# Kernel tuning notes

Measured on AMD Instinct MI355X. Metric: run time of the kernel, lower is better.

## Reference

```python
import jax, jax.numpy as jnp
import numpy as np

L0, L1, L2, L3 = 300000, 60000, 15000, 4000
E0, E1, E2 = 960000, 240000, 64000
F_IN, F_HID, F_OUT = 256, 128, 47


def setup_inputs() -> dict:
    key = jax.random.key(0)
    ks = jax.random.split(key, 12)
    return {
        "features": jax.random.normal(ks[0], (L0, F_IN), dtype=jnp.float32),
        "src0": jax.random.randint(ks[1], (E0,), 0, L0, dtype=jnp.int32),
        "dst0": jax.random.randint(ks[2], (E0,), 0, L1, dtype=jnp.int32),
        "src1": jax.random.randint(ks[3], (E1,), 0, L1, dtype=jnp.int32),
        "dst1": jax.random.randint(ks[4], (E1,), 0, L2, dtype=jnp.int32),
        "src2": jax.random.randint(ks[5], (E2,), 0, L2, dtype=jnp.int32),
        "dst2": jax.random.randint(ks[6], (E2,), 0, L3, dtype=jnp.int32),
        "W1": jax.random.normal(ks[7], (F_IN, F_HID), dtype=jnp.float32) * (1.0 / np.sqrt(F_IN)),
        "b1": jnp.zeros((F_HID,), dtype=jnp.float32),
        "W2": jax.random.normal(ks[8], (F_HID, F_HID), dtype=jnp.float32) * (1.0 / np.sqrt(F_HID)),
        "b2": jnp.zeros((F_HID,), dtype=jnp.float32),
        "W3": jax.random.normal(ks[9], (F_HID, F_OUT), dtype=jnp.float32) * (1.0 / np.sqrt(F_HID)),
        "b3": jnpp if False else jnp.zeros((F_OUT,), dtype=jnp.float32),
    }


def mean_agg(h, src, dst, n_dst):
    # copy_src gather over edges, then segment-mean over dst nodes
    msg = h[src]                                              # [E, F]
    s = jax.ops.segment_sum(msg, dst, num_segments=n_dst)     # [n_dst, F]
    cnt = jax.ops.segment_sum(jnp.ones_like(dst, dtype=h.dtype), dst, num_segments=n_dst)
    return s / jnp.maximum(cnt, 1.0)[:, None]


def reference(features, src0, dst0, src1, dst1, src2, dst2, W1, b1, W2, b2, W3, b3):
    # layer 0 -> 1: mean agg + linear + relu
    h = jax.nn.relu(mean_agg(features, src0, dst0, L1) @ W1 + b1)
    # layer 1 -> 2: mean agg + linear + relu
    h = jax.nn.relu(mean_agg(h, src1, dst1, L2) @ W2 + b2)
    # layer 2 -> 3: mean agg + linear (no activation on output layer)
    h = mean_agg(h, src2, dst2, L3) @ W3 + b3
    return h
```

## Files before the change

### kernel.cpp

```cpp
#include <hip/hip_runtime.h>

#define NL0 300000
#define NL1 60000
#define NL2 15000
#define NL3 4000
#define NE0 960000
#define NE1 240000
#define NE2 64000
#define E_ALL (NE0 + NE1 + NE2)
#define F_IN 256
#define F_HID 128
#define F_OUT 47

#define RBASE1 NL1
#define RBASE2 (NL1 + NL2)
#define NROWS (NL1 + NL2 + NL3)

#define FILL_BLOCKS ((E_ALL + 255) / 256)
#define WPREP_BLOCKS ((F_IN * F_HID) / 256)

typedef __attribute__((ext_vector_type(8))) short short8v;
typedef __attribute__((ext_vector_type(4))) float f32x4;

__device__ inline int wave_incl_scan(int v) {
    int lane = threadIdx.x & 63;
#pragma unroll
    for (int off = 1; off < 64; off <<= 1) {
        int t = __shfl_up(v, off, 64);
        if (lane >= off) v += t;
    }
    return v;
}

__device__ inline void bf16_split(float x, unsigned short& hi, unsigned short& lo) {
    unsigned int u = __float_as_uint(x);
    hi = (unsigned short)(u >> 16);
    float fh = __uint_as_float(u & 0xffff0000u);
    float l = x - fh;
    lo = (unsigned short)(__float_as_uint(l) >> 16);
}

__global__ void histogram_all(const int* __restrict__ dst0, const int* __restrict__ dst1,
                              const int* __restrict__ dst2, int* __restrict__ cnt) {
    int i = blockIdx.x * blockDim.x + threadIdx.x;
    if (i >= E_ALL) return;
    int k;
    if (i < NE0) {
        k = dst0[i];
    } else if (i < NE0 + NE1) {
        k = RBASE1 + dst1[i - NE0];
    } else {
        k = RBASE2 + dst2[i - NE0 - NE1];
    }
    atomicAdd(&cnt[k], 1);
}

__global__ __launch_bounds__(1024) void scan_block(const int* __restrict__ cnt, int N,
                                                   int* __restrict__ row_start,
                                                   int* __restrict__ blocksum) {
    __shared__ int wsum[16];
    int i = blockIdx.x * 1024 + threadIdx.x;
    int lane = threadIdx.x & 63, wid = threadIdx.x >> 6;
    int v = (i < N) ? cnt[i] : 0;
    int incl = wave_incl_scan(v);
    if (lane == 63) wsum[wid] = incl;
    __syncthreads();
    if (threadIdx.x < 16) {
        int w = wsum[threadIdx.x];
#pragma unroll
        for (int off = 1; off < 16; off <<= 1) {
            int t = __shfl_up(w, off, 64);
            if ((int)threadIdx.x >= off) w += t;
        }
        wsum[threadIdx.x] = w;
    }
    __syncthreads();
    int woff = wid ? wsum[wid - 1] : 0;
    if (i < N) row_start[i] = woff + incl - v;
    if (threadIdx.x == 0) blocksum[blockIdx.x] = wsum[15];
}

__global__ __launch_bounds__(1024) void add_offsets2(int* __restrict__ row_start,
                                                     const int* __restrict__ bs, int N, int E,
                                                     int* __restrict__ cursor) {
    __shared__ int soff;
    if (threadIdx.x < 64) {
        int s = 0;
        for (int j = threadIdx.x; j < blockIdx.x; j += 64) s += bs[j];
#pragma unroll
        for (int o = 32; o >= 1; o >>= 1) s += __shfl_xor(s, o, 64);
        if (threadIdx.x == 0) soff = s;
    }
    __syncthreads();
    int i = blockIdx.x * 1024 + threadIdx.x;
    if (i < N) {
        int v = row_start[i] + soff;
        row_start[i] = v;
        cursor[i] = v;
    }
    if (i == 0) row_start[N] = E;
}

__global__ void fill_all(const int* __restrict__ src0, const int* __restrict__ dst0,
                         const int* __restrict__ src1, const int* __restrict__ dst1,
                         const int* __restrict__ src2, const int* __restrict__ dst2,
                         int* __restrict__ cursor, int* __restrict__ ss,
                         const float* __restrict__ W1,
                         unsigned short* __restrict__ Whi,
                         unsigned short* __restrict__ Wlo) {
    int b = blockIdx.x;
    if (b >= FILL_BLOCKS) {
        int idx = (b - FILL_BLOCKS) * 256 + threadIdx.x;
        int k = idx >> 7, c = idx & 127;
        unsigned short h, l;
        bf16_split(W1[idx], h, l);
        Whi[c * 256 + k] = h;
        Wlo[c * 256 + k] = l;
        return;
    }
    int i = b * 256 + threadIdx.x;
    if (i >= E_ALL) return;
    int k, s;
    if (i < NE0) {
        s = src0[i];
        k = dst0[i];
    } else if (i < NE0 + NE1) {
        int e = i - NE0;
        s = src1[e];
        k = RBASE1 + dst1[e];
    } else {
        int e = i - NE0 - NE1;
        s = src2[e];
        k = RBASE2 + dst2[e];
    }
    int p = atomicAdd(&cursor[k], 1);
    ss[p] = s;
}

__global__ __launch_bounds__(256) void gather256(const float* __restrict__ h,
                                                 const int* __restrict__ rs,
                                                 const int* __restrict__ ss,
                                                 unsigned short* __restrict__ mhi,
                                                 unsigned short* __restrict__ mlo) {
    int lane = threadIdx.x & 63;
    int r = blockIdx.x * 4 + (threadIdx.x >> 6);
    if (r >= NL1) return;
    int s0 = rs[r], s1 = rs[r + 1];
    int tot = s1 - s0;

    const float* hp = h + (size_t)lane * 4;
    float4 acc0 = make_float4(0.f, 0.f, 0.f, 0.f);
    float4 acc1 = make_float4(0.f, 0.f, 0.f, 0.f);
    int e = s0;
    for (; e + 7 < s1; e += 8) {
        int i0 = ss[e], i1 = ss[e + 1], i2 = ss[e + 2], i3 = ss[e + 3];
        int i4 = ss[e + 4], i5 = ss[e + 5], i6 = ss[e + 6], i7 = ss[e + 7];
        float4 v0 = *(const float4*)(hp + (size_t)i0 * F_IN);
        float4 v1 = *(const float4*)(hp + (size_t)i1 * F_IN);
        float4 v2 = *(const float4*)(hp + (size_t)i2 * F_IN);
        float4 v3 = *(const float4*)(hp + (size_t)i3 * F_IN);
        float4 v4 = *(const float4*)(hp + (size_t)i4 * F_IN);
        float4 v5 = *(const float4*)(hp + (size_t)i5 * F_IN);
        float4 v6 = *(const float4*)(hp + (size_t)i6 * F_IN);
        float4 v7 = *(const float4*)(hp + (size_t)i7 * F_IN);
        acc0.x += (v0.x + v1.x) + (v2.x + v3.x);
        acc0.y += (v0.y + v1.y) + (v2.y + v3.y);
        acc0.z += (v0.z + v1.z) + (v2.z + v3.z);
        acc0.w += (v0.w + v1.w) + (v2.w + v3.w);
        acc1.x += (v4.x + v5.x) + (v6.x + v7.x);
        acc1.y += (v4.y + v5.y) + (v6.y + v7.y);
        acc1.z += (v4.z + v5.z) + (v6.z + v7.z);
        acc1.w += (v4.w + v5.w) + (v6.w + v7.w);
    }
    for (; e + 1 < s1; e += 2) {
        int i0 = ss[e], i1 = ss[e + 1];
        float4 v0 = *(const float4*)(hp + (size_t)i0 * F_IN);
        float4 v1 = *(const float4*)(hp + (size_t)i1 * F_IN);
        acc0.x += v0.x + v1.x; acc0.y += v0.y + v1.y;
        acc0.z += v0.z + v1.z; acc0.w += v0.w + v1.w;
    }
    if (e < s1) {
        int i0 = ss[e];
        float4 v0 = *(const float4*)(hp + (size_t)i0 * F_IN);
        acc0.x += v0.x; acc0.y += v0.y; acc0.z += v0.z; acc0.w += v0.w;
    }
    float inv = (tot > 0) ? 1.0f / (float)tot : 0.0f;
    float o[4] = {(acc0.x + acc1.x) * inv, (acc0.y + acc1.y) * inv,
                  (acc0.z + acc1.z) * inv, (acc0.w + acc1.w) * inv};
    ushort4 hv, lv;
    bf16_split(o[0], hv.x, lv.x);
    bf16_split(o[1], hv.y, lv.y);
    bf16_split(o[2], hv.z, lv.z);
    bf16_split(o[3], hv.w, lv.w);
    *(ushort4*)(mhi + (size_t)r * F_IN + lane * 4) = hv;
    *(ushort4*)(mlo + (size_t)r * F_IN + lane * 4) = lv;
}

__global__ __launch_bounds__(1024) void mfma_lin0(const unsigned short* __restrict__ Ahi,
                                                  const unsigned short* __restrict__ Alo,
                                                  const unsigned short* __restrict__ Whi,
                                                  const unsigned short* __restrict__ Wlo,
                                                  const float* __restrict__ bias,
                                                  float* __restrict__ out, int N) {
    __shared__ unsigned short whi[F_IN * F_HID];
    __shared__ unsigned short wlo[F_IN * F_HID];

    for (int ci = threadIdx.x; ci < (F_IN * F_HID) / 8; ci += 1024) {
        int e = ci * 8;
        int c = e >> 8;
        int swz = e ^ ((c & 7) << 3);
        *(short8v*)(whi + swz) = *(const short8v*)(Whi + e);
        *(short8v*)(wlo + swz) = *(const short8v*)(Wlo + e);
    }
    __syncthreads();

    int lane = threadIdx.x & 63;
    int wid = threadIdx.x >> 6;
    int rowbase = blockIdx.x * 256 + wid * 16;
    int r = lane & 15;
    int kg = lane >> 4;

    size_t arow = (size_t)min(rowbase + r, N - 1);
    const unsigned short* pah = Ahi + arow * F_IN + kg * 8;
    const unsigned short* pal = Alo + arow * F_IN + kg * 8;

    f32x4 acc[8];
#pragma unroll
    for (int ct = 0; ct < 8; ++ct) acc[ct] = (f32x4){0.f, 0.f, 0.f, 0.f};

#pragma unroll
    for (int ks = 0; ks < 8; ++ks) {
        short8v ah = *(const short8v*)(pah + ks * 32);
        short8v al = *(const short8v*)(pal + ks * 32);
#pragma unroll
        for (int ct = 0; ct < 8; ++ct) {
            int e = (((ct * 16 + r) << 8) + ks * 32 + kg * 8) ^ ((r & 7) << 3);
            short8v bh = *(const short8v*)(whi + e);
            short8v bl = *(const short8v*)(wlo + e);
            acc[ct] = __builtin_amdgcn_mfma_f32_16x16x32_bf16(ah, bh, acc[ct], 0, 0, 0);
            acc[ct] = __builtin_amdgcn_mfma_f32_16x16x32_bf16(ah, bl, acc[ct], 0, 0, 0);
            acc[ct] = __builtin_amdgcn_mfma_f32_16x16x32_bf16(al, bh, acc[ct], 0, 0, 0);
        }
    }

    int crow = rowbase + kg * 4;
#pragma unroll
    for (int ct = 0; ct < 8; ++ct) {
        float bb = bias[ct * 16 + r];
#pragma unroll
        for (int i = 0; i < 4; ++i) {
            int rr = crow + i;
            if (rr < N) out[(size_t)rr * F_HID + ct * 16 + r] = fmaxf(acc[ct][i] + bb, 0.f);
        }
    }
}

template <int FOUT, int ROWS, bool RELU>
__global__ __launch_bounds__(256) void gather_linear(const float* __restrict__ h,
                                                     const int* __restrict__ rs,
                                                     const int* __restrict__ ss,
                                                     const float* __restrict__ W,
                                                     const float* __restrict__ bias,
                                                     float* __restrict__ out,
                                                     int N, int rowbase) {
    __shared__ float mr[ROWS][128];

    int lane = threadIdx.x & 63;
    int w = threadIdx.x >> 6;
    int half = lane >> 5;
    int hl = lane & 31;
    int rb = blockIdx.x * ROWS;
    constexpr int RPW = ROWS / 4;
#pragma unroll
    for (int q = 0; q < RPW; ++q) {
        int lr = w * RPW + q;
        int r = rb + lr;
        float4 acc = make_float4(0.f, 0.f, 0.f, 0.f);
        if (r < N) {
            int s0 = rs[rowbase + r], s1 = rs[rowbase + r + 1];
            const float* hp = h + (size_t)hl * 4;
            int e = s0;
            for (; e + 3 < s1; e += 4) {
                int i0 = ss[e + half], i1 = ss[e + 2 + half];
                float4 v0 = *(const float4*)(hp + (size_t)i0 * F_HID);
                float4 v1 = *(const float4*)(hp + (size_t)i1 * F_HID);
                acc.x += v0.x + v1.x; acc.y += v0.y + v1.y;
                acc.z += v0.z + v1.z; acc.w += v0.w + v1.w;
            }
            if (e + 1 < s1) {
                int i0 = ss[e + half];
                float4 v0 = *(const float4*)(hp + (size_t)i0 * F_HID);
                acc.x += v0.x; acc.y += v0.y; acc.z += v0.z; acc.w += v0.w;
                e += 2;
            }
            if (e < s1 && half == 0) {
                int i0 = ss[e];
                float4 v0 = *(const float4*)(hp + (size_t)i0 * F_HID);
                acc.x += v0.x; acc.y += v0.y; acc.z += v0.z; acc.w += v0.w;
            }
            acc.x += __shfl(acc.x, lane ^ 32);
            acc.y += __shfl(acc.y, lane ^ 32);
            acc.z += __shfl(acc.z, lane ^ 32);
            acc.w += __shfl(acc.w, lane ^ 32);
            float inv = (s1 > s0) ? 1.0f / (float)(s1 - s0) : 0.0f;
            acc.x *= inv; acc.y *= inv; acc.z *= inv; acc.w *= inv;
        }
        if (half == 0) *(float4*)&mr[lr][hl * 4] = acc;
    }
    __syncthreads();

    if constexpr (FOUT == 128) {
        int c4 = (threadIdx.x & 31) * 4;
        int r0 = (threadIdx.x >> 5) & 7;
        float4 bb = *(const float4*)&bias[c4];
        float4 a0 = bb, a1 = bb;
#pragma unroll 8
        for (int k = 0; k < 128; ++k) {
            float4 wv = *(const float4*)&W[k * 128 + c4];
            float m0 = mr[r0][k];
            float m1 = mr[r0 + 8][k];
            a0.x += m0 * wv.x; a0.y += m0 * wv.y; a0.z += m0 * wv.z; a0.w += m0 * wv.w;
            a1.x += m1 * wv.x; a1.y += m1 * wv.y; a1.z += m1 * wv.z; a1.w += m1 * wv.w;
        }
        if (RELU) {
            a0.x = fmaxf(a0.x, 0.f); a0.y = fmaxf(a0.y, 0.f);
            a0.z = fmaxf(a0.z, 0.f); a0.w = fmaxf(a0.w, 0.f);
            a1.x = fmaxf(a1.x, 0.f); a1.y = fmaxf(a1.y, 0.f);
            a1.z = fmaxf(a1.z, 0.f); a1.w = fmaxf(a1.w, 0.f);
        }
        int ra = rb + r0, rb2 = rb + r0 + 8;
        if (ra < N) *(float4*)&out[(size_t)ra * 128 + c4] = a0;
        if (rb2 < N) *(float4*)&out[(size_t)rb2 * 128 + c4] = a1;
    } else {
        int j = lane;
        int rg = w;
        if (j < FOUT) {
            float bb = bias[j];
            float a0 = bb, a1 = bb;
#pragma unroll 8
            for (int k = 0; k < 128; ++k) {
                float wv = W[k * FOUT + j];
                a0 += mr[rg][k] * wv;
                a1 += mr[rg + 4][k] * wv;
            }
            if (RELU) { a0 = fmaxf(a0, 0.f); a1 = fmaxf(a1, 0.f); }
            int ra = rb + rg, rb2 = rb + rg + 4;
            if (ra < N) out[(size_t)ra * FOUT + j] = a0;
            if (rb2 < N) out[(size_t)rb2 * FOUT + j] = a1;
        }
    }
}


static inline size_t align256(size_t x) { return (x + 255) & ~size_t(255); }

extern "C" void kernel_launch(void* const* d_in, const int* in_sizes, int n_in,
                              void* d_out, int out_size, void* d_ws, size_t ws_size,
                              hipStream_t stream) {
    const float* features = (const float*)d_in[0];
    const int*   src0     = (const int*)d_in[1];
    const int*   dst0     = (const int*)d_in[2];
    const int*   src1     = (const int*)d_in[3];
    const int*   dst1     = (const int*)d_in[4];
    const int*   src2     = (const int*)d_in[5];
    const int*   dst2     = (const int*)d_in[6];
    const float* W1       = (const float*)d_in[7];
    const float* b1       = (const float*)d_in[8];
    const float* W2       = (const float*)d_in[9];
    const float* b2       = (const float*)d_in[10];
    const float* W3       = (const float*)d_in[11];
    const float* b3       = (const float*)d_in[12];
    float* out = (float*)d_out;

    char* p = (char*)d_ws;
    size_t off = 0;
    auto alloc = [&](size_t bytes) {
        char* r = p + off;
        off += align256(bytes);
        return r;
    };
    unsigned short* m0hi = (unsigned short*)alloc(sizeof(unsigned short) * (size_t)NL1 * F_IN);
    unsigned short* m0lo = (unsigned short*)alloc(sizeof(unsigned short) * (size_t)NL1 * F_IN);
    unsigned short* wt_hi = (unsigned short*)alloc(sizeof(unsigned short) * F_IN * F_HID);
    unsigned short* wt_lo = (unsigned short*)alloc(sizeof(unsigned short) * F_IN * F_HID);
    float* h1 = (float*)alloc(sizeof(float) * (size_t)NL1 * F_HID);
    float* h2 = (float*)alloc(sizeof(float) * (size_t)NL2 * F_HID);
    int* cnt = (int*)alloc(sizeof(int) * NROWS);
    int* rs  = (int*)alloc(sizeof(int) * (NROWS + 1));
    int* cur = (int*)alloc(sizeof(int) * NROWS);
    int* bs  = (int*)alloc(sizeof(int) * 1024);
    int* ss  = (int*)alloc(sizeof(int) * E_ALL);
    (void)ws_size;

    hipMemsetAsync(cnt, 0, sizeof(int) * NROWS, stream);
    histogram_all<<<(E_ALL + 255) / 256, 256, 0, stream>>>(dst0, dst1, dst2, cnt);
    int nb = (NROWS + 1023) / 1024;
    scan_block<<<nb, 1024, 0, stream>>>(cnt, NROWS, rs, bs);
    add_offsets2<<<nb, 1024, 0, stream>>>(rs, bs, NROWS, E_ALL, cur);
    fill_all<<<FILL_BLOCKS + WPREP_BLOCKS, 256, 0, stream>>>(
        src0, dst0, src1, dst1, src2, dst2, cur, ss, W1, wt_hi, wt_lo);

    gather256<<<NL1 / 4, 256, 0, stream>>>(features, rs, ss, m0hi, m0lo);
    mfma_lin0<<<(NL1 + 255) / 256, 1024, 0, stream>>>(m0hi, m0lo, wt_hi, wt_lo, b1, h1, NL1);

    gather_linear<128, 16, true><<<(NL2 + 15) / 16, 256, 0, stream>>>(
        h1, rs, ss, W2, b2, h2, NL2, RBASE1);

    gather_linear<F_OUT, 8, false><<<(NL3 + 7) / 8, 256, 0, stream>>>(
        h2, rs, ss, W3, b3, out, NL3, RBASE2);
}
```

Measured before the change: 372.7 us.

## Build CSR with partitioned counters and precomputed ranks instead of atomic fill

Replaces the histogram plus atomic-cursor fill with a count pass that records each edge's rank within one of eight per-partition counters, then places edges deterministically from per-partition bases. This removes the second round of atomics in the fill kernel and spreads counter contention across eight copies. In exchange it adds an 8x larger counter array to memset and scan, an extra rank array of E_ALL ints to write and read, and more reads in the scan and offset kernels. A relu statement reorder is also included.

```diff
diff --git a/kernel.cpp b/kernel.cpp
--- a/kernel.cpp
+++ b/kernel.cpp
@@ -16,6 +16,7 @@
 #define RBASE2 (NL1 + NL2)
 #define NROWS (NL1 + NL2 + NL3)
 
+#define NPART 8
 #define FILL_BLOCKS ((E_ALL + 255) / 256)
 #define WPREP_BLOCKS ((F_IN * F_HID) / 256)
 
@@ -40,28 +41,34 @@
     lo = (unsigned short)(__float_as_uint(l) >> 16);
 }
 
-__global__ void histogram_all(const int* __restrict__ dst0, const int* __restrict__ dst1,
-                              const int* __restrict__ dst2, int* __restrict__ cnt) {
-    int i = blockIdx.x * blockDim.x + threadIdx.x;
+__device__ inline int edge_row(int i, const int* __restrict__ dst0,
+                               const int* __restrict__ dst1, const int* __restrict__ dst2) {
+    if (i < NE0) return dst0[i];
+    if (i < NE0 + NE1) return RBASE1 + dst1[i - NE0];
+    return RBASE2 + dst2[i - NE0 - NE1];
+}
+
+__global__ void count_rank(const int* __restrict__ dst0, const int* __restrict__ dst1,
+                           const int* __restrict__ dst2,
+                           int* __restrict__ cnt8, int* __restrict__ rank) {
+    int i = blockIdx.x * 256 + threadIdx.x;
     if (i >= E_ALL) return;
-    int k;
-    if (i < NE0) {
-        k = dst0[i];
-    } else if (i < NE0 + NE1) {
-        k = RBASE1 + dst1[i - NE0];
-    } else {
-        k = RBASE2 + dst2[i - NE0 - NE1];
-    }
-    atomicAdd(&cnt[k], 1);
-}
-
-__global__ __launch_bounds__(1024) void scan_block(const int* __restrict__ cnt, int N,
-                                                   int* __restrict__ row_start,
-                                                   int* __restrict__ blocksum) {
+    int k = edge_row(i, dst0, dst1, dst2);
+    int part = blockIdx.x & (NPART - 1);
+    rank[i] = atomicAdd(&cnt8[part * NROWS + k], 1);
+}
+
+__global__ __launch_bounds__(1024) void scan_block8(const int* __restrict__ cnt8,
+                                                    int* __restrict__ row_start,
+                                                    int* __restrict__ blocksum) {
     __shared__ int wsum[16];
     int i = blockIdx.x * 1024 + threadIdx.x;
     int lane = threadIdx.x & 63, wid = threadIdx.x >> 6;
-    int v = (i < N) ? cnt[i] : 0;
+    int v = 0;
+    if (i < NROWS) {
+#pragma unroll
+        for (int p = 0; p < NPART; ++p) v += cnt8[p * NROWS + i];
+    }
     int incl = wave_incl_scan(v);
     if (lane == 63) wsum[wid] = incl;
     __syncthreads();
@@ -76,13 +83,14 @@
     }
     __syncthreads();
     int woff = wid ? wsum[wid - 1] : 0;
-    if (i < N) row_start[i] = woff + incl - v;
+    if (i < NROWS) row_start[i] = woff + incl - v;
     if (threadIdx.x == 0) blocksum[blockIdx.x] = wsum[15];
 }
 
-__global__ __launch_bounds__(1024) void add_offsets2(int* __restrict__ row_start,
-                                                     const int* __restrict__ bs, int N, int E,
-                                                     int* __restrict__ cursor) {
+__global__ __launch_bounds__(1024) void add_offsets8(int* __restrict__ row_start,
+                                                     const int* __restrict__ bs,
+                                                     const int* __restrict__ cnt8,
+                                                     int* __restrict__ pbase) {
     __shared__ int soff;
     if (threadIdx.x < 64) {
         int s = 0;
@@ -93,21 +101,27 @@
     }
     __syncthreads();
     int i = blockIdx.x * 1024 + threadIdx.x;
-    if (i < N) {
+    if (i < NROWS) {
         int v = row_start[i] + soff;
         row_start[i] = v;
-        cursor[i] = v;
-    }
-    if (i == 0) row_start[N] = E;
-}
-
-__global__ void fill_all(const int* __restrict__ src0, const int* __restrict__ dst0,
-                         const int* __restrict__ src1, const int* __restrict__ dst1,
-                         const int* __restrict__ src2, const int* __restrict__ dst2,
-                         int* __restrict__ cursor, int* __restrict__ ss,
-                         const float* __restrict__ W1,
-                         unsigned short* __restrict__ Whi,
-                         unsigned short* __restrict__ Wlo) {
+        int running = v;
+#pragma unroll
+        for (int p = 0; p < NPART; ++p) {
+            pbase[p * NROWS + i] = running;
+            running += cnt8[p * NROWS + i];
+        }
+    }
+    if (i == 0) row_start[NROWS] = E_ALL;
+}
+
+__global__ void place_all(const int* __restrict__ src0, const int* __restrict__ dst0,
+                          const int* __restrict__ src1, const int* __restrict__ dst1,
+                          const int* __restrict__ src2, const int* __restrict__ dst2,
+                          const int* __restrict__ pbase, const int* __restrict__ rank,
+                          int* __restrict__ ss,
+                          const float* __restrict__ W1,
+                          unsigned short* __restrict__ Whi,
+                          unsigned short* __restrict__ Wlo) {
     int b = blockIdx.x;
     if (b >= FILL_BLOCKS) {
         int idx = (b - FILL_BLOCKS) * 256 + threadIdx.x;
@@ -120,21 +134,10 @@
     }
     int i = b * 256 + threadIdx.x;
     if (i >= E_ALL) return;
-    int k, s;
-    if (i < NE0) {
-        s = src0[i];
-        k = dst0[i];
-    } else if (i < NE0 + NE1) {
-        int e = i - NE0;
-        s = src1[e];
-        k = RBASE1 + dst1[e];
-    } else {
-        int e = i - NE0 - NE1;
-        s = src2[e];
-        k = RBASE2 + dst2[e];
-    }
-    int p = atomicAdd(&cursor[k], 1);
-    ss[p] = s;
+    int k = edge_row(i, dst0, dst1, dst2);
+    int s = (i < NE0) ? src0[i] : (i < NE0 + NE1) ? src1[i - NE0] : src2[i - NE0 - NE1];
+    int part = b & (NPART - 1);
+    ss[pbase[part * NROWS + k] + rank[i]] = s;
 }
 
 __global__ __launch_bounds__(256) void gather256(const float* __restrict__ h,
@@ -326,7 +329,7 @@
             a0.x = fmaxf(a0.x, 0.f); a0.y = fmaxf(a0.y, 0.f);
             a0.z = fmaxf(a0.z, 0.f); a0.w = fmaxf(a0.w, 0.f);
             a1.x = fmaxf(a1.x, 0.f); a1.y = fmaxf(a1.y, 0.f);
-            a1.z = fmaxf(a1.z, 0.f); a1.w = fmaxf(a1.w, 0.f);
+            a1.w = fmaxf(a1.w, 0.f); a1.z = fmaxf(a1.z, 0.f);
         }
         int ra = rb + r0, rb2 = rb + r0 + 8;
         if (ra < N) *(float4*)&out[(size_t)ra * 128 + c4] = a0;
@@ -385,20 +388,21 @@
     unsigned short* wt_lo = (unsigned short*)alloc(sizeof(unsigned short) * F_IN * F_HID);
     float* h1 = (float*)alloc(sizeof(float) * (size_t)NL1 * F_HID);
     float* h2 = (float*)alloc(sizeof(float) * (size_t)NL2 * F_HID);
-    int* cnt = (int*)alloc(sizeof(int) * NROWS);
-    int* rs  = (int*)alloc(sizeof(int) * (NROWS + 1));
-    int* cur = (int*)alloc(sizeof(int) * NROWS);
-    int* bs  = (int*)alloc(sizeof(int) * 1024);
-    int* ss  = (int*)alloc(sizeof(int) * E_ALL);
+    int* cnt8  = (int*)alloc(sizeof(int) * NPART * NROWS);
+    int* pbase = (int*)alloc(sizeof(int) * NPART * NROWS);
+    int* rank  = (int*)alloc(sizeof(int) * E_ALL);
+    int* rs    = (int*)alloc(sizeof(int) * (NROWS + 1));
+    int* bs    = (int*)alloc(sizeof(int) * 1024);
+    int* ss    = (int*)alloc(sizeof(int) * E_ALL);
     (void)ws_size;
 
-    hipMemsetAsync(cnt, 0, sizeof(int) * NROWS, stream);
-    histogram_all<<<(E_ALL + 255) / 256, 256, 0, stream>>>(dst0, dst1, dst2, cnt);
+    hipMemsetAsync(cnt8, 0, sizeof(int) * NPART * NROWS, stream);
+    count_rank<<<FILL_BLOCKS, 256, 0, stream>>>(dst0, dst1, dst2, cnt8, rank);
     int nb = (NROWS + 1023) / 1024;
-    scan_block<<<nb, 1024, 0, stream>>>(cnt, NROWS, rs, bs);
-    add_offsets2<<<nb, 1024, 0, stream>>>(rs, bs, NROWS, E_ALL, cur);
-    fill_all<<<FILL_BLOCKS + WPREP_BLOCKS, 256, 0, stream>>>(
-        src0, dst0, src1, dst1, src2, dst2, cur, ss, W1, wt_hi, wt_lo);
+    scan_block8<<<nb, 1024, 0, stream>>>(cnt8, rs, bs);
+    add_offsets8<<<nb, 1024, 0, stream>>>(rs, bs, cnt8, pbase);
+    place_all<<<FILL_BLOCKS + WPREP_BLOCKS, 256, 0, stream>>>(
+        src0, dst0, src1, dst1, src2, dst2, pbase, rank, ss, W1, wt_hi, wt_lo);
 
     gather256<<<NL1 / 4, 256, 0, stream>>>(features, rs, ss, m0hi, m0lo);
     mfma_lin0<<<(NL1 + 255) / 256, 1024, 0, stream>>>(m0hi, m0lo, wt_hi, wt_lo, b1, h1, NL1);
```

After: 317.9 us. -14.7%, faster.
